# Kernel optimization log

Hardware: AMD Instinct MI355X
Metric: run time of the kernel (lower is better)

Reference implementation:

```python
import jax, jax.numpy as jnp
import numpy as np

D_MODEL = 1024
SCALE = 1.0 / np.sqrt(D_MODEL).astype(np.float32)


def setup_inputs() -> dict:
    key = jax.random.key(0)
    ks = jax.random.split(key, 9)
    B, S, D = 4, 2048, D_MODEL
    init = 1.0 / np.sqrt(D).astype(np.float32)
    return {
        "q": jax.random.normal(ks[0], (B, S, D), jnp.float32),
        "k": jax.random.normal(ks[1], (B, S, D), jnp.float32),
        "v": jax.random.normal(ks[2], (B, S, D), jnp.float32),
        "Wq": jax.random.uniform(ks[3], (D, D), jnp.float32, -init, init),
        "bq": jax.random.uniform(ks[4], (D,), jnp.float32, -init, init),
        "Wk": jax.random.uniform(ks[5], (D, D), jnp.float32, -init, init),
        "bk": jax.random.uniform(ks[6], (D,), jnp.float32, -init, init),
        "Wv": jax.random.uniform(ks[7], (D, D), jnp.float32, -init, init),
        "bv": jax.random.uniform(ks[8], (D,), jnp.float32, -init, init),
    }


def reference(q, k, v, Wq, bq, Wk, bk, Wv, bv):
    # Linear projections (torch Linear: x @ W.T + b)
    qp = jnp.einsum('bsd,ed->bse', q, Wq) + bq
    kp = jnp.einsum('bsd,ed->bse', k, Wk) + bk
    vp = jnp.einsum('bsd,ed->bse', v, Wv) + bv
    qp = jax.nn.softmax(qp, axis=-1)          # softmax over feature dim
    kp = jax.nn.softmax(kp, axis=-2) * SCALE  # softmax over sequence dim
    vp = jax.nn.softmax(vp, axis=-2)          # softmax over sequence dim
    attn_weights = jnp.einsum('bqd,bkd->bqk', qp, kp)  # [B,S,S]
    output = jnp.einsum('bqk,bkd->bqd', attn_weights, vp)
    return (output, attn_weights)
```

## Files before the change

kernel.cpp:

```cpp
#include <hip/hip_runtime.h>
#include <math.h>


typedef float  f32x4  __attribute__((ext_vector_type(4)));
typedef __bf16 bf16x8 __attribute__((ext_vector_type(8)));
typedef int    i32x4  __attribute__((ext_vector_type(4)));
typedef unsigned short u16;

__device__ __forceinline__ float b2f(u16 u) {
    unsigned int i = ((unsigned int)u) << 16; float f;
    __builtin_memcpy(&f, &i, 4); return f;
}
__device__ __forceinline__ u16 f2b(float f) {
    unsigned int i; __builtin_memcpy(&i, &f, 4);
    i += 0x7FFFu + ((i >> 16) & 1u);
    return (u16)(i >> 16);
}

__global__ __launch_bounds__(256) void cvt_all(
    const float4* __restrict__ q, const float4* __restrict__ k,
    const float4* __restrict__ v, const float4* __restrict__ Wq,
    const float4* __restrict__ Wk, const float4* __restrict__ Wv,
    const float* __restrict__ bq, const float* __restrict__ bk,
    const float* __restrict__ bv,
    ushort4* __restrict__ qb, ushort4* __restrict__ kb,
    ushort4* __restrict__ vb, ushort4* __restrict__ Wb,
    float* __restrict__ biasCat)
{
    int bid = blockIdx.x, t = threadIdx.x;
    const float4* s; ushort4* d; int idx;
    if (bid < 8192)       { s = q;  d = qb;            idx = bid * 256 + t; }
    else if (bid < 16384) { s = k;  d = kb;            idx = (bid - 8192) * 256 + t; }
    else if (bid < 24576) { s = v;  d = vb;            idx = (bid - 16384) * 256 + t; }
    else if (bid < 25600) { s = Wq; d = Wb;            idx = (bid - 24576) * 256 + t; }
    else if (bid < 26624) { s = Wk; d = Wb + 262144;   idx = (bid - 25600) * 256 + t; }
    else if (bid < 27648) { s = Wv; d = Wb + 524288;   idx = (bid - 26624) * 256 + t; }
    else {
        for (int i = t; i < 3072; i += 256)
            biasCat[i] = (i < 1024) ? bq[i] : (i < 2048) ? bk[i - 1024] : bv[i - 2048];
        return;
    }
    float4 vv = s[idx];
    ushort4 o;
    o.x = f2b(vv.x); o.y = f2b(vv.y); o.z = f2b(vv.z); o.w = f2b(vv.w);
    d[idx] = o;
}

__global__ __launch_bounds__(512, 2) void gemm256_attn(
    const u16* __restrict__ Ap, const u16* __restrict__ Bp,
    float* __restrict__ C32, u16* __restrict__ C16,
    int N, int K, long long sA, long long sB, long long sC)
{
    __shared__ __align__(16) u16 lds[65536];

    const int tid  = threadIdx.x;
    const int lane = tid & 63;
    const int w    = tid >> 6;
    const int wr   = w >> 2, wc = w & 3;

    const int gx  = gridDim.x;
    const int tot = gx * gridDim.y;
    const int lin = blockIdx.y * gx + blockIdx.x;
    const int vlin = (lin & 7) * (tot >> 3) + (lin >> 3);
    const int bx = vlin % gx, by = vlin / gx;
    const int m0 = by * 256, n0 = bx * 256;
    const int z  = blockIdx.z;

    const u16* Ag = Ap + (size_t)z * sA;
    const u16* Bg = Bp + (size_t)z * sB;

    const int cl = tid ^ ((tid >> 4) & 6);
    const int lr = cl >> 3;
    const int ce = (cl & 7) * 8;
    const int arow = m0 + lr;
    const int brow = n0 + (lr & 31) + ((lr & 32) << 1);

    const int axr = ((lane >> 2) & 3) << 4;
    const int ar0 = (wr * 64 + (lane & 15)) * 64 + (lane >> 4) * 8;
    const int br0 = (wc * 32 + (lane & 15)) * 64 + (lane >> 4) * 8;

#define GLL16(gsrc, ldsoff)                                                    \
    __builtin_amdgcn_global_load_lds(                                          \
        (__attribute__((address_space(1))) void*)(uintptr_t)(gsrc),            \
        (__attribute__((address_space(3))) void*)&lds[ldsoff], 16, 0, 0)

#define STAGE_A(c, h, T)                                                       \
    do { const u16* _s = Ag + (size_t)(arow + (h) * 64) * K + (T) * 64 + ce;   \
         int _d = (((c) << 1) + (h)) * 8192 + tid * 8;                         \
         GLL16(_s, _d); GLL16(_s + (size_t)128 * K, _d + 4096); } while (0)

#define STAGE_B(c, g, T)                                                       \
    do { const u16* _s = Bg + (size_t)(brow + (g) * 32) * K + (T) * 64 + ce;   \
         int _d = 32768 + (((c) << 1) + (g)) * 8192 + tid * 8;                 \
         GLL16(_s, _d); GLL16(_s + (size_t)128 * K, _d + 4096); } while (0)

#define SBAR asm volatile("s_barrier" ::: "memory")
#define LGKM0 do { asm volatile("s_waitcnt lgkmcnt(0)" ::: "memory");          \
                   __builtin_amdgcn_sched_barrier(0); } while (0)

#define LDA(base)                                                              \
    _Pragma("unroll") for (int mi2 = 0; mi2 < 4; ++mi2)                        \
    _Pragma("unroll") for (int ks = 0; ks < 2; ++ks)                           \
        afr[mi2][ks] = __builtin_bit_cast(bf16x8,                              \
            *(const i32x4*)&lds[(base) + ((ar0 + mi2 * 1024 + ks * 32) ^ axr)]);

#define LDB(dst, base)                                                         \
    _Pragma("unroll") for (int ni2 = 0; ni2 < 2; ++ni2)                        \
    _Pragma("unroll") for (int ks = 0; ks < 2; ++ks)                           \
        dst[ni2][ks] = __builtin_bit_cast(bf16x8,                              \
            *(const i32x4*)&lds[(base) + ((br0 + ni2 * 1024 + ks * 32) ^ axr)]);

#define MFMA_Q(mb, nb, bfrag)                                                  \
    __builtin_amdgcn_s_setprio(1);                                             \
    _Pragma("unroll") for (int mi2 = 0; mi2 < 4; ++mi2)                        \
    _Pragma("unroll") for (int ni2 = 0; ni2 < 2; ++ni2)                        \
    _Pragma("unroll") for (int ks = 0; ks < 2; ++ks)                           \
        acc[(mb) + mi2][(nb) + ni2] = __builtin_amdgcn_mfma_f32_16x16x32_bf16( \
            afr[mi2][ks], bfrag[ni2][ks], acc[(mb) + mi2][(nb) + ni2], 0, 0, 0); \
    __builtin_amdgcn_s_setprio(0)

    f32x4 acc[8][4];
#pragma unroll
    for (int i = 0; i < 8; ++i)
#pragma unroll
        for (int j = 0; j < 4; ++j) acc[i][j] = (f32x4)0.0f;

    bf16x8 afr[4][2], b0f[2][2], b1f[2][2];

    const int nt = K >> 6;

    STAGE_A(0, 0, 0); STAGE_B(0, 0, 0);
    STAGE_A(0, 1, 0); STAGE_B(0, 1, 0);
    STAGE_A(1, 0, 1); STAGE_B(1, 0, 1);

    for (int T = 0; T < nt; ++T) {
        const int cur = T & 1, nxt = cur ^ 1;
        const int ab = (cur << 1) * 8192;
        const int bb = 32768 + (cur << 1) * 8192;

        if (T + 1 < nt) asm volatile("s_waitcnt vmcnt(4)" ::: "memory");
        else            asm volatile("s_waitcnt vmcnt(0)" ::: "memory");
        SBAR;
        LDA(ab); LDB(b0f, bb);
        if (T + 1 < nt) STAGE_B(nxt, 1, T + 1);
        SBAR; LGKM0;
        MFMA_Q(0, 0, b0f);
        SBAR;
        LDB(b1f, bb + 8192);
        if (T + 1 < nt) STAGE_A(nxt, 1, T + 1);
        SBAR; LGKM0;
        MFMA_Q(0, 2, b1f);
        SBAR;
        LDA(ab + 8192);
        if (T + 2 < nt) STAGE_A(cur, 0, T + 2);
        SBAR; LGKM0;
        MFMA_Q(4, 0, b0f);
        SBAR;
        if (T + 2 < nt) STAGE_B(cur, 0, T + 2);
        SBAR; LGKM0;
        MFMA_Q(4, 2, b1f);
        SBAR;
    }

    const int cr0 = m0 + wr * 128 + ((lane >> 4) << 2);
    const int cc0 = n0 + wc * 64 + (lane & 15);
    float* Cg = C32 + (size_t)z * sC;
#pragma unroll
    for (int mi = 0; mi < 8; ++mi)
#pragma unroll
        for (int ni = 0; ni < 4; ++ni)
#pragma unroll
            for (int j = 0; j < 4; ++j)
                Cg[(size_t)(cr0 + mi * 16 + j) * N + cc0 + ni * 16] = acc[mi][ni][j];

    u16* sE = lds;
    u16* Cb = C16 + (size_t)z * sC;
    const int wrow0 = ((lane >> 4) << 2);
    const int wcol0 = wc * 64 + (lane & 15);
    const int rr = tid >> 2;
    const int c0 = (tid & 3) * 8;
    __syncthreads();
#pragma unroll
    for (int p = 0; p < 2; ++p) {
        if (wr == p) {
#pragma unroll
            for (int mi = 0; mi < 8; ++mi)
#pragma unroll
                for (int ni = 0; ni < 4; ++ni)
#pragma unroll
                    for (int j = 0; j < 4; ++j)
                        sE[(wrow0 + mi * 16 + j) * 264 + wcol0 + ni * 16] =
                            f2b(acc[mi][ni][j]);
        }
        __syncthreads();
#pragma unroll
        for (int i = 0; i < 8; ++i) {
            i32x4 vv = *(const i32x4*)&sE[rr * 264 + c0 + i * 32];
            *(i32x4*)&Cb[(size_t)(m0 + p * 128 + rr) * N + n0 + c0 + i * 32] = vv;
        }
        if (p == 0) __syncthreads();
    }
#undef GLL16
#undef STAGE_A
#undef STAGE_B
#undef LDA
#undef LDB
#undef MFMA_Q
}

template<int EPI>
__global__ __launch_bounds__(512, 4) void gemm128(
    const u16* __restrict__ Ap, const u16* __restrict__ Bp,
    float* __restrict__ C32, u16* __restrict__ C16, u16* __restrict__ Calt,
    const float* __restrict__ bias,
    int N, int K, long long sA, long long sB, long long sC)
{
    __shared__ __align__(16) u16 lds[32768];

    const int tid  = threadIdx.x;
    const int lane = tid & 63;
    const int w    = tid >> 6;
    const int wr   = w >> 2, wc = w & 3;

    const int gx  = gridDim.x;
    const int tot = gx * gridDim.y;
    const int lin = blockIdx.y * gx + blockIdx.x;
    const int vlin = (lin & 7) * (tot >> 3) + (lin >> 3);
    const int bx = vlin % gx, by = vlin / gx;
    const int m0 = by * 128, n0 = bx * 128;
    const int z  = blockIdx.z;

    const u16* Ag = Ap + (size_t)z * sA;
    const u16* Bg = Bp + (size_t)z * sB;

    const int cl = tid ^ ((tid >> 3) & 3);
    const int lr = cl >> 2;
    const int ce = (cl & 3) * 8;
    const int arow = m0 + lr, brow = n0 + lr;

    const int exr = ((lane >> 1) & 3) << 3;
    const int ar0 = (wr * 64 + (lane & 15)) * 32 + (lane >> 4) * 8;
    const int br0 = (wc * 32 + (lane & 15)) * 32 + (lane >> 4) * 8;

#define GLL16(gsrc, ldsoff)                                                    \
    __builtin_amdgcn_global_load_lds(                                          \
        (__attribute__((address_space(1))) void*)(uintptr_t)(gsrc),            \
        (__attribute__((address_space(3))) void*)&lds[ldsoff], 16, 0, 0)

#define STAGE_A(c, h, T)                                                       \
    GLL16(Ag + (size_t)arow * K + (T) * 64 + (h) * 32 + ce,                    \
          (((c) << 1) + (h)) * 4096 + tid * 8)

#define STAGE_B(c, h, T)                                                       \
    GLL16(Bg + (size_t)brow * K + (T) * 64 + (h) * 32 + ce,                    \
          16384 + (((c) << 1) + (h)) * 4096 + tid * 8)

#define LGKM0 do { asm volatile("s_waitcnt lgkmcnt(0)" ::: "memory");          \
                   __builtin_amdgcn_sched_barrier(0); } while (0)

#define LDAB(base)                                                             \
    _Pragma("unroll") for (int mi2 = 0; mi2 < 4; ++mi2)                        \
        afr[mi2] = __builtin_bit_cast(bf16x8,                                  \
            *(const i32x4*)&lds[(base) + ((ar0 + mi2 * 512) ^ exr)]);          \
    _Pragma("unroll") for (int ni2 = 0; ni2 < 2; ++ni2)                        \
        bfr[ni2] = __builtin_bit_cast(bf16x8,                                  \
            *(const i32x4*)&lds[16384 + (base) + ((br0 + ni2 * 512) ^ exr)]);

#define MFMA8                                                                  \
    __builtin_amdgcn_s_setprio(1);                                             \
    _Pragma("unroll") for (int mi2 = 0; mi2 < 4; ++mi2)                        \
    _Pragma("unroll") for (int ni2 = 0; ni2 < 2; ++ni2)                        \
        acc[mi2][ni2] = __builtin_amdgcn_mfma_f32_16x16x32_bf16(               \
            afr[mi2], bfr[ni2], acc[mi2][ni2], 0, 0, 0);                       \
    __builtin_amdgcn_s_setprio(0)

    f32x4 acc[4][2];
#pragma unroll
    for (int i = 0; i < 4; ++i)
#pragma unroll
        for (int j = 0; j < 2; ++j) acc[i][j] = (f32x4)0.0f;

    bf16x8 afr[4], bfr[2];

    const int nt = K >> 6;

    STAGE_A(0, 0, 0); STAGE_B(0, 0, 0);
    STAGE_A(0, 1, 0); STAGE_B(0, 1, 0);
    STAGE_A(1, 0, 1); STAGE_B(1, 0, 1);

    for (int T = 0; T < nt; ++T) {
        const int cur = T & 1, nxt = cur ^ 1;
        const int ab = (cur << 1) * 4096;

        if (T + 1 < nt) asm volatile("s_waitcnt vmcnt(4)" ::: "memory");
        else            asm volatile("s_waitcnt vmcnt(2)" ::: "memory");
        asm volatile("s_barrier" ::: "memory");
        LDAB(ab);
        if (T + 1 < nt) { STAGE_A(nxt, 1, T + 1); STAGE_B(nxt, 1, T + 1); }
        LGKM0;
        MFMA8;

        if (T + 1 < nt) asm volatile("s_waitcnt vmcnt(4)" ::: "memory");
        else            asm volatile("s_waitcnt vmcnt(0)" ::: "memory");
        asm volatile("s_barrier" ::: "memory");
        LDAB(ab + 4096);
        if (T + 2 < nt) { STAGE_A(cur, 0, T + 2); STAGE_B(cur, 0, T + 2); }
        LGKM0;
        MFMA8;
    }

    if constexpr (EPI == 1) {
        u16* sE = lds;
        u16* Cb = (z == 2) ? Calt : (C16 + (size_t)z * sC);
        const int colb = wc * 32 + (lane & 15);
        float bv0 = bias[(size_t)z * 1024 + n0 + colb];
        float bv1 = bias[(size_t)z * 1024 + n0 + colb + 16];
        const int wrow0 = wr * 64 + ((lane >> 4) << 2);
        __syncthreads();
#pragma unroll
        for (int mi = 0; mi < 4; ++mi)
#pragma unroll
            for (int j = 0; j < 4; ++j) {
                int row = wrow0 + mi * 16 + j;
                sE[row * 136 + colb]      = f2b(__expf(acc[mi][0][j] + bv0));
                sE[row * 136 + colb + 16] = f2b(__expf(acc[mi][1][j] + bv1));
            }
        __syncthreads();
        const int rr = tid >> 2, c0 = (tid & 3) * 8;
#pragma unroll
        for (int i = 0; i < 4; ++i) {
            i32x4 vv = *(const i32x4*)&sE[rr * 136 + c0 + i * 32];
            *(i32x4*)&Cb[(size_t)(m0 + rr) * N + n0 + c0 + i * 32] = vv;
        }
    } else {
        float* Cg = C32 + (size_t)z * sC;
        const int cr0 = m0 + wr * 64 + ((lane >> 4) << 2);
        const int cc0 = n0 + wc * 32 + (lane & 15);
#pragma unroll
        for (int mi = 0; mi < 4; ++mi)
#pragma unroll
            for (int ni = 0; ni < 2; ++ni)
#pragma unroll
                for (int j = 0; j < 4; ++j)
                    Cg[(size_t)(cr0 + mi * 16 + j) * N + cc0 + ni * 16] =
                        acc[mi][ni][j];
    }
#undef GLL16
#undef STAGE_A
#undef STAGE_B
#undef LGKM0
#undef LDAB
#undef MFMA8
}

__global__ __launch_bounds__(256) void sm_partials(
    u16* __restrict__ qE, const u16* __restrict__ kE, const u16* __restrict__ vE,
    float* __restrict__ kpart, float* __restrict__ vpart)
{
    int bid = blockIdx.x, t = threadIdx.x;
    if (bid < 8192) {
        u16* p = qE + (size_t)bid * 1024;
        ushort4 v = *(ushort4*)&p[t * 4];
        float e0 = b2f(v.x), e1 = b2f(v.y), e2 = b2f(v.z), e3 = b2f(v.w);
        float s = (e0 + e1) + (e2 + e3);
#pragma unroll
        for (int off = 32; off; off >>= 1) s += __shfl_down(s, off);
        __shared__ float red[4];
        if ((t & 63) == 0) red[t >> 6] = s;
        __syncthreads();
        float inv = 1.0f / ((red[0] + red[1]) + (red[2] + red[3]));
        ushort4 o;
        o.x = f2b(e0 * inv); o.y = f2b(e1 * inv);
        o.z = f2b(e2 * inv); o.w = f2b(e3 * inv);
        *(ushort4*)&p[t * 4] = o;
    } else {
        int j = bid - 8192;
        const u16* d; float* part;
        if (j < 64) { d = kE; part = kpart; } else { d = vE; part = vpart; j -= 64; }
        int b = j >> 4, c = j & 15;
        const u16* base = d + ((size_t)b * 2048 + c * 128) * 1024 + t * 4;
        float a0 = 0, a1 = 0, a2 = 0, a3 = 0;
        for (int s = 0; s < 128; ++s) {
            ushort4 v = *(const ushort4*)(base + (size_t)s * 1024);
            a0 += b2f(v.x); a1 += b2f(v.y); a2 += b2f(v.z); a3 += b2f(v.w);
        }
        *(float4*)(part + ((size_t)(b * 16 + c)) * 1024 + t * 4) = make_float4(a0, a1, a2, a3);
    }
}

__global__ __launch_bounds__(256) void col_reduce2(
    const float* __restrict__ kpart, const float* __restrict__ vpart,
    float* __restrict__ kinv, float* __restrict__ vinv)
{
    int bid = blockIdx.x;
    const float* part; float* inv; float mult;
    if (bid < 16) { part = kpart; inv = kinv; mult = 0.03125f; }
    else          { part = vpart; inv = vinv; mult = 1.0f; bid -= 16; }
    int idx = bid * 256 + threadIdx.x;
    int b = idx >> 10, e = idx & 1023;
    float s = 0;
    for (int c = 0; c < 16; ++c) s += part[((size_t)(b * 16 + c)) * 1024 + e];
    inv[idx] = mult / s;
}

__global__ __launch_bounds__(256) void norm_all(
    u16* __restrict__ kE, const float* __restrict__ kinv,
    const u16* __restrict__ vE, const float* __restrict__ vinv,
    u16* __restrict__ vpT)
{
    int bid = blockIdx.x, t = threadIdx.x;
    if (bid < 8192) {
        int b = bid >> 11, s = bid & 2047;
        u16* p = kE + ((size_t)b * 2048 + s) * 1024 + t * 4;
        float4 iv = *(const float4*)(kinv + b * 1024 + t * 4);
        ushort4 v = *(ushort4*)p;
        v.x = f2b(b2f(v.x) * iv.x); v.y = f2b(b2f(v.y) * iv.y);
        v.z = f2b(b2f(v.z) * iv.z); v.w = f2b(b2f(v.w) * iv.w);
        *(ushort4*)p = v;
    } else {
        __shared__ __align__(16) u16 tile[64][68];
        int j = bid - 8192;
        int b = j >> 9, y = (j >> 5) & 15, x = j & 31;
        int s0 = x * 64, e0 = y * 64;
        int lr = t >> 4, lc = (t & 15) * 4;
#pragma unroll
        for (int i = 0; i < 4; ++i) {
            int sr = i * 16 + lr;
            ushort4 v = *(const ushort4*)(vE + ((size_t)b * 2048 + s0 + sr) * 1024 + e0 + lc);
            tile[sr][lc] = v.x; tile[sr][lc + 1] = v.y;
            tile[sr][lc + 2] = v.z; tile[sr][lc + 3] = v.w;
        }
        __syncthreads();
#pragma unroll
        for (int i = 0; i < 4; ++i) {
            int er = i * 16 + lr;
            float iv = vinv[b * 1024 + e0 + er];
            ushort4 v;
            v.x = f2b(b2f(tile[lc + 0][er]) * iv);
            v.y = f2b(b2f(tile[lc + 1][er]) * iv);
            v.z = f2b(b2f(tile[lc + 2][er]) * iv);
            v.w = f2b(b2f(tile[lc + 3][er]) * iv);
            *(ushort4*)(vpT + ((size_t)b * 1024 + e0 + er) * 2048 + s0 + lc) = v;
        }
    }
}

extern "C" void kernel_launch(void* const* d_in, const int* in_sizes, int n_in,
                              void* d_out, int out_size, void* d_ws, size_t ws_size,
                              hipStream_t stream)
{
    const float* q  = (const float*)d_in[0];
    const float* k  = (const float*)d_in[1];
    const float* v  = (const float*)d_in[2];
    const float* Wq = (const float*)d_in[3];
    const float* bq = (const float*)d_in[4];
    const float* Wk = (const float*)d_in[5];
    const float* bk = (const float*)d_in[6];
    const float* Wv = (const float*)d_in[7];
    const float* bv = (const float*)d_in[8];

    float* out  = (float*)d_out;
    float* attn = out + 8388608;

    u16* wsU = (u16*)d_ws;
    u16* qE   = wsU;
    u16* kE   = wsU + 8388608;
    u16* Wb   = wsU + 16777216;
    u16* qb   = wsU + 25165824;
    u16* kb   = wsU + 33554432;
    u16* vb   = wsU + 41943040;
    u16* vpT  = wsU + 25165824;
    u16* attnB = wsU + 33554432;
    u16* vE   = (u16*)attn;

    float* tail  = (float*)(wsU + 50331648);
    float* kpart = tail;
    float* vpart = tail + 65536;
    float* kinv  = tail + 131072;
    float* vinv  = tail + 135168;
    float* biasCat = tail + 139264;

    const long long SD = 2048LL * 1024, SS = 2048LL * 2048, DS = 1024LL * 2048;

    cvt_all<<<dim3(27649), dim3(256), 0, stream>>>(
        (const float4*)q, (const float4*)k, (const float4*)v,
        (const float4*)Wq, (const float4*)Wk, (const float4*)Wv,
        bq, bk, bv,
        (ushort4*)qb, (ushort4*)kb, (ushort4*)vb, (ushort4*)Wb, biasCat);

    gemm128<1><<<dim3(8, 64, 3), dim3(512), 0, stream>>>(
        qb, Wb, nullptr, qE, vE, biasCat,
        1024, 1024, 8388608LL, 1048576LL, 8388608LL);

    sm_partials<<<dim3(8320), dim3(256), 0, stream>>>(qE, kE, vE, kpart, vpart);

    col_reduce2<<<dim3(32), dim3(256), 0, stream>>>(kpart, vpart, kinv, vinv);

    norm_all<<<dim3(10240), dim3(256), 0, stream>>>(kE, kinv, vE, vinv, vpT);

    gemm256_attn<<<dim3(8, 8, 4), dim3(512), 0, stream>>>(
        qE, kE, attn, attnB, 2048, 1024, SD, SD, SS);

    gemm128<2><<<dim3(8, 16, 4), dim3(512), 0, stream>>>(
        attnB, vpT, out, nullptr, nullptr, nullptr, 1024, 2048, SS, DS, SD);
}
```

Measured before the change: 221.4 us.

## Replace gemm128 with 4-wave triple-buffered GEMM using larger per-warp tiles

Replaces the 8-wave 128x128 GEMM with a templated 4-wave kernel whose warp tiles grow from 64x32 to (BM/2)x64. It uses a K-step of 32 with a three-buffer LDS ring that keeps two tiles in flight. The projection GEMM now uses 256x128 block tiles, halving its grid, while the final attn@V GEMM keeps 128x128. The aim is more MFMA work per LDS fragment load and fewer barriers per FLOP. The cost is higher register pressure (up to 32 accumulators per lane at BM=256), fewer waves for latency hiding, and a smaller grid for the projection.

Result: faster. 215.7 us (-2.5%).

```diff
diff --git a/kernel.cpp b/kernel.cpp
--- a/kernel.cpp
+++ b/kernel.cpp
@@ -208,149 +208,148 @@
 #undef MFMA_Q
 }
 
-template<int EPI>
-__global__ __launch_bounds__(512, 4) void gemm128(
+template<int EPI, int BM>
+__global__ __launch_bounds__(256, 2) void gemm_bw(
     const u16* __restrict__ Ap, const u16* __restrict__ Bp,
     float* __restrict__ C32, u16* __restrict__ C16, u16* __restrict__ Calt,
     const float* __restrict__ bias,
     int N, int K, long long sA, long long sB, long long sC)
 {
-    __shared__ __align__(16) u16 lds[32768];
+    constexpr int AMI = BM / 32;
+    constexpr int ALD = BM / 64;
+    constexpr int ASZ = BM * 32;
+    constexpr int BUF = ASZ + 4096;
+    __shared__ __align__(16) u16 lds[3 * BUF];
 
     const int tid  = threadIdx.x;
     const int lane = tid & 63;
     const int w    = tid >> 6;
-    const int wr   = w >> 2, wc = w & 3;
+    const int wr   = w >> 1, wc = w & 1;
 
     const int gx  = gridDim.x;
     const int tot = gx * gridDim.y;
     const int lin = blockIdx.y * gx + blockIdx.x;
     const int vlin = (lin & 7) * (tot >> 3) + (lin >> 3);
     const int bx = vlin % gx, by = vlin / gx;
-    const int m0 = by * 128, n0 = bx * 128;
+    const int m0 = by * BM, n0 = bx * 128;
     const int z  = blockIdx.z;
 
     const u16* Ag = Ap + (size_t)z * sA;
     const u16* Bg = Bp + (size_t)z * sB;
 
-    const int cl = tid ^ ((tid >> 3) & 3);
-    const int lr = cl >> 2;
-    const int ce = (cl & 3) * 8;
-    const int arow = m0 + lr, brow = n0 + lr;
+    const int cltid = tid ^ ((tid >> 3) & 3);
+    const int crow  = cltid >> 2;
+    const int ce    = (cltid & 3) * 8;
 
     const int exr = ((lane >> 1) & 3) << 3;
-    const int ar0 = (wr * 64 + (lane & 15)) * 32 + (lane >> 4) * 8;
-    const int br0 = (wc * 32 + (lane & 15)) * 32 + (lane >> 4) * 8;
-
-#define GLL16(gsrc, ldsoff)                                                    \
+    const int ar0 = (wr * (BM / 2) + (lane & 15)) * 32 + (lane >> 4) * 8;
+    const int br0 = (wc * 64 + (lane & 15)) * 32 + (lane >> 4) * 8;
+
+#define GLLW(gsrc, ldsoff)                                                     \
     __builtin_amdgcn_global_load_lds(                                          \
         (__attribute__((address_space(1))) void*)(uintptr_t)(gsrc),            \
         (__attribute__((address_space(3))) void*)&lds[ldsoff], 16, 0, 0)
 
-#define STAGE_A(c, h, T)                                                       \
-    GLL16(Ag + (size_t)arow * K + (T) * 64 + (h) * 32 + ce,                    \
-          (((c) << 1) + (h)) * 4096 + tid * 8)
-
-#define STAGE_B(c, h, T)                                                       \
-    GLL16(Bg + (size_t)brow * K + (T) * 64 + (h) * 32 + ce,                    \
-          16384 + (((c) << 1) + (h)) * 4096 + tid * 8)
-
-#define LGKM0 do { asm volatile("s_waitcnt lgkmcnt(0)" ::: "memory");          \
-                   __builtin_amdgcn_sched_barrier(0); } while (0)
-
-#define LDAB(base)                                                             \
-    _Pragma("unroll") for (int mi2 = 0; mi2 < 4; ++mi2)                        \
-        afr[mi2] = __builtin_bit_cast(bf16x8,                                  \
-            *(const i32x4*)&lds[(base) + ((ar0 + mi2 * 512) ^ exr)]);          \
-    _Pragma("unroll") for (int ni2 = 0; ni2 < 2; ++ni2)                        \
-        bfr[ni2] = __builtin_bit_cast(bf16x8,                                  \
-            *(const i32x4*)&lds[16384 + (base) + ((br0 + ni2 * 512) ^ exr)]);
-
-#define MFMA8                                                                  \
-    __builtin_amdgcn_s_setprio(1);                                             \
-    _Pragma("unroll") for (int mi2 = 0; mi2 < 4; ++mi2)                        \
-    _Pragma("unroll") for (int ni2 = 0; ni2 < 2; ++ni2)                        \
-        acc[mi2][ni2] = __builtin_amdgcn_mfma_f32_16x16x32_bf16(               \
-            afr[mi2], bfr[ni2], acc[mi2][ni2], 0, 0, 0);                       \
-    __builtin_amdgcn_s_setprio(0)
-
-    f32x4 acc[4][2];
-#pragma unroll
-    for (int i = 0; i < 4; ++i)
-#pragma unroll
-        for (int j = 0; j < 2; ++j) acc[i][j] = (f32x4)0.0f;
-
-    bf16x8 afr[4], bfr[2];
-
-    const int nt = K >> 6;
-
-    STAGE_A(0, 0, 0); STAGE_B(0, 0, 0);
-    STAGE_A(0, 1, 0); STAGE_B(0, 1, 0);
-    STAGE_A(1, 0, 1); STAGE_B(1, 0, 1);
+#define STAGE(buf, T)                                                          \
+    do {                                                                       \
+        _Pragma("unroll") for (int ld = 0; ld < ALD; ++ld)                     \
+            GLLW(Ag + (size_t)(m0 + ld * 64 + crow) * K + (T) * 32 + ce,       \
+                 (buf) + ld * 2048 + tid * 8);                                 \
+        _Pragma("unroll") for (int ld = 0; ld < 2; ++ld)                       \
+            GLLW(Bg + (size_t)(n0 + ld * 64 + crow) * K + (T) * 32 + ce,       \
+                 (buf) + ASZ + ld * 2048 + tid * 8);                           \
+    } while (0)
+
+#define LGKM0B do { asm volatile("s_waitcnt lgkmcnt(0)" ::: "memory");         \
+                    __builtin_amdgcn_sched_barrier(0); } while (0)
+
+    f32x4 acc[AMI][4];
+#pragma unroll
+    for (int i = 0; i < AMI; ++i)
+#pragma unroll
+        for (int j = 0; j < 4; ++j) acc[i][j] = (f32x4)0.0f;
+
+    bf16x8 afr[AMI], bfr[4];
+
+    const int nt = K >> 5;
+
+    int b0 = 0, b1 = BUF, b2 = 2 * BUF;
+    STAGE(b0, 0); STAGE(b1, 1);
 
     for (int T = 0; T < nt; ++T) {
-        const int cur = T & 1, nxt = cur ^ 1;
-        const int ab = (cur << 1) * 4096;
-
-        if (T + 1 < nt) asm volatile("s_waitcnt vmcnt(4)" ::: "memory");
-        else            asm volatile("s_waitcnt vmcnt(2)" ::: "memory");
+        if (T + 1 < nt) {
+            if constexpr (BM == 256) asm volatile("s_waitcnt vmcnt(6)" ::: "memory");
+            else                     asm volatile("s_waitcnt vmcnt(4)" ::: "memory");
+        } else {
+            asm volatile("s_waitcnt vmcnt(0)" ::: "memory");
+        }
         asm volatile("s_barrier" ::: "memory");
-        LDAB(ab);
-        if (T + 1 < nt) { STAGE_A(nxt, 1, T + 1); STAGE_B(nxt, 1, T + 1); }
-        LGKM0;
-        MFMA8;
-
-        if (T + 1 < nt) asm volatile("s_waitcnt vmcnt(4)" ::: "memory");
-        else            asm volatile("s_waitcnt vmcnt(0)" ::: "memory");
-        asm volatile("s_barrier" ::: "memory");
-        LDAB(ab + 4096);
-        if (T + 2 < nt) { STAGE_A(cur, 0, T + 2); STAGE_B(cur, 0, T + 2); }
-        LGKM0;
-        MFMA8;
+#pragma unroll
+        for (int mi = 0; mi < AMI; ++mi)
+            afr[mi] = __builtin_bit_cast(bf16x8,
+                *(const i32x4*)&lds[b0 + ((ar0 + mi * 512) ^ exr)]);
+#pragma unroll
+        for (int ni = 0; ni < 4; ++ni)
+            bfr[ni] = __builtin_bit_cast(bf16x8,
+                *(const i32x4*)&lds[b0 + ASZ + ((br0 + ni * 512) ^ exr)]);
+        if (T + 2 < nt) STAGE(b2, T + 2);
+        LGKM0B;
+        __builtin_amdgcn_s_setprio(1);
+#pragma unroll
+        for (int mi = 0; mi < AMI; ++mi)
+#pragma unroll
+            for (int ni = 0; ni < 4; ++ni)
+                acc[mi][ni] = __builtin_amdgcn_mfma_f32_16x16x32_bf16(
+                    afr[mi], bfr[ni], acc[mi][ni], 0, 0, 0);
+        __builtin_amdgcn_s_setprio(0);
+        int tmp = b0; b0 = b1; b1 = b2; b2 = tmp;
     }
 
     if constexpr (EPI == 1) {
         u16* sE = lds;
         u16* Cb = (z == 2) ? Calt : (C16 + (size_t)z * sC);
-        const int colb = wc * 32 + (lane & 15);
-        float bv0 = bias[(size_t)z * 1024 + n0 + colb];
-        float bv1 = bias[(size_t)z * 1024 + n0 + colb + 16];
-        const int wrow0 = wr * 64 + ((lane >> 4) << 2);
+        const int colb = wc * 64 + (lane & 15);
+        float bv[4];
+#pragma unroll
+        for (int ni = 0; ni < 4; ++ni)
+            bv[ni] = bias[(size_t)z * 1024 + n0 + colb + ni * 16];
+        const int wrow0 = wr * (BM / 2) + ((lane >> 4) << 2);
         __syncthreads();
 #pragma unroll
-        for (int mi = 0; mi < 4; ++mi)
-#pragma unroll
-            for (int j = 0; j < 4; ++j) {
-                int row = wrow0 + mi * 16 + j;
-                sE[row * 136 + colb]      = f2b(__expf(acc[mi][0][j] + bv0));
-                sE[row * 136 + colb + 16] = f2b(__expf(acc[mi][1][j] + bv1));
-            }
+        for (int mi = 0; mi < AMI; ++mi)
+#pragma unroll
+            for (int ni = 0; ni < 4; ++ni)
+#pragma unroll
+                for (int j = 0; j < 4; ++j)
+                    sE[(wrow0 + mi * 16 + j) * 136 + colb + ni * 16] =
+                        f2b(__expf(acc[mi][ni][j] + bv[ni]));
         __syncthreads();
         const int rr = tid >> 2, c0 = (tid & 3) * 8;
 #pragma unroll
-        for (int i = 0; i < 4; ++i) {
-            i32x4 vv = *(const i32x4*)&sE[rr * 136 + c0 + i * 32];
-            *(i32x4*)&Cb[(size_t)(m0 + rr) * N + n0 + c0 + i * 32] = vv;
+        for (int rb = 0; rb < BM / 64; ++rb) {
+            int row = rb * 64 + rr;
+#pragma unroll
+            for (int i = 0; i < 4; ++i) {
+                i32x4 vv = *(const i32x4*)&sE[row * 136 + c0 + i * 32];
+                *(i32x4*)&Cb[(size_t)(m0 + row) * N + n0 + c0 + i * 32] = vv;
+            }
         }
     } else {
         float* Cg = C32 + (size_t)z * sC;
-        const int cr0 = m0 + wr * 64 + ((lane >> 4) << 2);
-        const int cc0 = n0 + wc * 32 + (lane & 15);
-#pragma unroll
-        for (int mi = 0; mi < 4; ++mi)
-#pragma unroll
-            for (int ni = 0; ni < 2; ++ni)
+        const int cr0 = m0 + wr * (BM / 2) + ((lane >> 4) << 2);
+        const int cc0 = n0 + wc * 64 + (lane & 15);
+#pragma unroll
+        for (int mi = 0; mi < AMI; ++mi)
+#pragma unroll
+            for (int ni = 0; ni < 4; ++ni)
 #pragma unroll
                 for (int j = 0; j < 4; ++j)
                     Cg[(size_t)(cr0 + mi * 16 + j) * N + cc0 + ni * 16] =
                         acc[mi][ni][j];
     }
-#undef GLL16
-#undef STAGE_A
-#undef STAGE_B
-#undef LGKM0
-#undef LDAB
-#undef MFMA8
+#undef GLLW
+#undef STAGE
+#undef LGKM0B
 }
 
 __global__ __launch_bounds__(256) void sm_partials(
@@ -488,7 +487,7 @@
         bq, bk, bv,
         (ushort4*)qb, (ushort4*)kb, (ushort4*)vb, (ushort4*)Wb, biasCat);
 
-    gemm128<1><<<dim3(8, 64, 3), dim3(512), 0, stream>>>(
+    gemm_bw<1, 256><<<dim3(8, 32, 3), dim3(256), 0, stream>>>(
         qb, Wb, nullptr, qE, vE, biasCat,
         1024, 1024, 8388608LL, 1048576LL, 8388608LL);
 
@@ -501,6 +500,6 @@
     gemm256_attn<<<dim3(8, 8, 4), dim3(512), 0, stream>>>(
         qE, kE, attn, attnB, 2048, 1024, SD, SD, SS);
 
-    gemm128<2><<<dim3(8, 16, 4), dim3(512), 0, stream>>>(
+    gemm_bw<2, 128><<<dim3(8, 16, 4), dim3(256), 0, stream>>>(
         attnB, vpT, out, nullptr, nullptr, nullptr, 1024, 2048, SS, DS, SD);
 }
```
